# Optimization experiments

Measured on AMD Instinct MI355X. Metric: run time of the kernel, lower is better.

Reference implementation:

```python
import jax, jax.numpy as jnp
import numpy as np

B, T, C, N = 64, 2048, 1, 128  # batch, max seq len, num_conjugates, num_tags


def setup_inputs() -> dict:
    key = jax.random.key(0)
    k1, k2, k3, k4, k5 = jax.random.split(key, 5)
    emissions = jax.random.normal(k1, (B, T, C, N), dtype=jnp.float32)
    # ragged lengths in [T//2, T], guaranteed >= 1
    token_sizes = jax.random.randint(k2, (B,), T // 2, T + 1, dtype=jnp.int32)
    # learned CRF parameters (torch init is zeros; use small random for a nontrivial baseline)
    transitions = 0.1 * jax.random.normal(k3, (1, C, N, N), dtype=jnp.float32)
    head_transitions = 0.1 * jax.random.normal(k4, (1, C, N), dtype=jnp.float32)
    last_transitions = 0.1 * jax.random.normal(k5, (1, C, N), dtype=jnp.float32)
    return {
        "emissions": emissions,
        "token_sizes": token_sizes,
        "transitions": transitions,
        "head_transitions": head_transitions,
        "last_transitions": last_transitions,
    }


def _log_partition(emissions, transitions, head_transitions, last_transitions, token_sizes):
    # emissions: [B, T, C, N]; transitions: [1, C, N, N]; head/last: [1, C, N]
    trans = transitions[0]  # [C, N, N]
    # alpha_0 = head_transitions (*) emissions[0] in the Log semiring
    alpha0 = head_transitions[0][None, :, :] + emissions[:, 0]  # [B, C, N]

    def step(alpha, inp):
        em_t, t = inp  # em_t: [B, C, N], t: scalar time index
        # Log-semiring matmul: logsumexp over previous tag
        new = jax.nn.logsumexp(alpha[:, :, :, None] + trans[None, :, :, :], axis=2) + em_t
        valid = (t < token_sizes)[:, None, None]  # mask padded steps (identity in semiring)
        return jnp.where(valid, new, alpha), None

    step = jax.checkpoint(step)
    xs = (jnp.swapaxes(emissions[:, 1:], 0, 1), jnp.arange(1, emissions.shape[1]))
    alpha, _ = jax.lax.scan(step, alpha0, xs)
    # terminate with last_transitions, reduce over final tag
    return jax.nn.logsumexp(alpha + last_transitions[0][None, :, :], axis=-1)  # [B, C]


def reference(emissions, token_sizes, transitions, head_transitions, last_transitions):
    return _log_partition(emissions, transitions, head_transitions, last_transitions, token_sizes)
```

## Files before the change

### kernel.cpp

```cpp
#include <hip/hip_runtime.h>
#include <stdint.h>

#define T_LEN 2048
#define B_TOT 64
#define N_TAG 128
#define MID 1024

typedef __attribute__((ext_vector_type(4))) float f32x4;
typedef __attribute__((ext_vector_type(8))) short bf16x8;
typedef __attribute__((ext_vector_type(4))) uint32_t u32x4;
typedef __attribute__((ext_vector_type(2))) uint32_t u32x2;

template <int S>
struct IC {
  static constexpr int value = S;
};

__device__ __align__(16) float g_alpha[B_TOT][N_TAG];
__device__ __align__(16) float g_v[B_TOT][N_TAG];
__device__ float g_Lf[B_TOT];
__device__ float g_Lb[B_TOT];

__device__ __forceinline__ uint32_t pack2_bf16(float a, float b) {
  uint32_t ua = __float_as_uint(a) + 0x8000u;
  uint32_t ub = __float_as_uint(b) + 0x8000u;
  return __builtin_amdgcn_perm(ua, ub, 0x03020706u);
}
__device__ __forceinline__ float bf_lo(uint32_t w) {
  return __uint_as_float(w << 16);
}
__device__ __forceinline__ float bf_hi(uint32_t w) {
  return __uint_as_float(w & 0xffff0000u);
}

__global__ __launch_bounds__(256) void eem_prepass(const float* __restrict__ em,
                                                   uint32_t* __restrict__ ws) {
  const int tid = blockIdx.x * blockDim.x + threadIdx.x;
  const int b = tid >> 15;
  const int rem = tid & 32767;
  const int t = rem >> 4;
  const int kk = rem & 15;
  const float4* src =
      (const float4*)(em + ((size_t)b * T_LEN + t) * N_TAG + kk * 8);
  const float4 p0 = src[0];
  const float4 p1 = src[1];
  u32x4 o;
  o[0] = pack2_bf16(__expf(p0.x), __expf(p0.y));
  o[1] = pack2_bf16(__expf(p0.z), __expf(p0.w));
  o[2] = pack2_bf16(__expf(p1.x), __expf(p1.y));
  o[3] = pack2_bf16(__expf(p1.z), __expf(p1.w));
  *(u32x4*)(ws + ((size_t)t * B_TOT + b) * (N_TAG / 2) + kk * 4) = o;
}

__global__ __launch_bounds__(512, 2) void crf_scan_kernel(
    const float* __restrict__ em, const int* __restrict__ lens,
    const float* __restrict__ trans, const float* __restrict__ head,
    const float* __restrict__ last, const uint32_t* __restrict__ eem) {
  const int lane = threadIdx.x & 63;
  const int w = threadIdx.x >> 6;
  const int f = w >> 1;
  const int h = w & 1;
  const int c = lane & 15;
  const int q = lane >> 4;
  const bool is_fwd = (blockIdx.x < 4);
  const int bg = ((int)blockIdx.x & 3) * 16 + c;
  const int jbase = f * 32 + q * 8 + h * 4;

  __shared__ uint32_t x_lds[2][4][64][4];
  __shared__ int k_lds[16];

  const size_t eoff = (size_t)bg * 64 + f * 16 + q * 4 + h * 2;
  u32x2 eslot[4];
  auto issue_eem = [&](auto sc, int row) {
    constexpr int S = decltype(sc)::value;
    eslot[S] = *(const u32x2*)(eem + (size_t)row * 4096 + eoff);
  };

  const f32x4 vzero = {0.f, 0.f, 0.f, 0.f};

  if (is_fwd) {
    bf16x8 efrag[4];
    {
      const int j = f * 32 + (c >> 2) * 8 + h * 4 + (c & 3);
#pragma unroll
      for (int ktv = 0; ktv < 4; ++ktv) {
        const int ktp = (w + ktv) & 3;
        u32x4 wd;
#pragma unroll
        for (int p = 0; p < 4; ++p) {
          const int i0 = ktp * 32 + q * 8 + 2 * p;
          wd[p] = pack2_bf16(__expf(trans[(i0 + 0) * N_TAG + j]),
                             __expf(trans[(i0 + 1) * N_TAG + j]));
        }
        efrag[ktv] = __builtin_bit_cast(bf16x8, wd);
      }
    }
    float L = 0.f;
    const float* emb = em + (size_t)bg * T_LEN * N_TAG;
    {
      float v0[4];
#pragma unroll
      for (int r = 0; r < 4; ++r)
        v0[r] = __expf(head[jbase + r] + emb[jbase + r]);
      u32x2 wd;
      wd[0] = pack2_bf16(v0[0], v0[1]);
      wd[1] = pack2_bf16(v0[2], v0[3]);
      *(u32x2*)&x_lds[0][f][lane][h * 2] = wd;
    }
    if (w == 0 && lane < 16) k_lds[lane] = 0;
    __syncthreads();

    issue_eem(IC<1>{}, 1);
    issue_eem(IC<2>{}, 2);
    issue_eem(IC<3>{}, 3);

    auto step = [&](auto slotc, int t) {
      constexpr int SLOT = decltype(slotc)::value;
      constexpr int RP = (SLOT + 1) & 1;
      constexpr int WP = SLOT & 1;
      {
        int row = t + 3;
        if (row > T_LEN - 1) row = T_LEN - 1;
        issue_eem(IC<(SLOT + 3) & 3>{}, row);
      }
      int e = 0;
      if (SLOT == 1) e = k_lds[c];
      u32x4 bfr[4];
#pragma unroll
      for (int ktv = 0; ktv < 4; ++ktv)
        bfr[ktv] = *(const u32x4*)&x_lds[RP][(w + ktv) & 3][lane][0];
      const u32x2 ev = eslot[SLOT];
      float ff[4];
      ff[0] = bf_lo(ev[0]);
      ff[1] = bf_hi(ev[0]);
      ff[2] = bf_lo(ev[1]);
      ff[3] = bf_hi(ev[1]);
      if (SLOT == 1) {
        const float sc = __uint_as_float((uint32_t)(127 - e) << 23);
#pragma unroll
        for (int r = 0; r < 4; ++r) ff[r] *= sc;
        L += (float)e * 0.6931471805599453f;
      }
      f32x4 acc = __builtin_amdgcn_mfma_f32_16x16x32_bf16(
          efrag[0], __builtin_bit_cast(bf16x8, bfr[0]), vzero, 0, 0, 0);
      acc = __builtin_amdgcn_mfma_f32_16x16x32_bf16(
          efrag[1], __builtin_bit_cast(bf16x8, bfr[1]), acc, 0, 0, 0);
      acc = __builtin_amdgcn_mfma_f32_16x16x32_bf16(
          efrag[2], __builtin_bit_cast(bf16x8, bfr[2]), acc, 0, 0, 0);
      acc = __builtin_amdgcn_mfma_f32_16x16x32_bf16(
          efrag[3], __builtin_bit_cast(bf16x8, bfr[3]), acc, 0, 0, 0);
      if (SLOT == 0) {
        if (w == 0 && lane < 16)
          k_lds[c] = (int)(__float_as_uint(acc[0]) >> 23) - 126;
      }
      if (t == MID - 1) {
#pragma unroll
        for (int r = 0; r < 4; ++r) g_alpha[bg][jbase + r] = acc[r] * ff[r];
        if (w == 0 && q == 0) g_Lf[bg] = L;
      }
      u32x2 wd;
      wd[0] = pack2_bf16(acc[0] * ff[0], acc[1] * ff[1]);
      wd[1] = pack2_bf16(acc[2] * ff[2], acc[3] * ff[3]);
      *(u32x2*)&x_lds[WP][f][lane][h * 2] = wd;
      __syncthreads();
    };

    int t = 1;
#pragma unroll 1
    for (int it = 0; it < 255; ++it) {
      step(IC<1>{}, t);
      step(IC<2>{}, t + 1);
      step(IC<3>{}, t + 2);
      step(IC<0>{}, t + 3);
      t += 4;
    }
    step(IC<1>{}, t);
    step(IC<2>{}, t + 1);
    step(IC<3>{}, t + 2);
  } else {
    bf16x8 efrag[4];
    {
      const int irow = f * 32 + (c >> 2) * 8 + h * 4 + (c & 3);
#pragma unroll
      for (int ktv = 0; ktv < 4; ++ktv) {
        const int ktp = (w + ktv) & 3;
        u32x4 wd;
#pragma unroll
        for (int p = 0; p < 4; ++p) {
          const int j0 = ktp * 32 + q * 8 + 2 * p;
          wd[p] = pack2_bf16(__expf(trans[irow * N_TAG + j0 + 0]),
                             __expf(trans[irow * N_TAG + j0 + 1]));
        }
        efrag[ktv] = __builtin_bit_cast(bf16x8, wd);
      }
    }
    const int mylen = lens[bg];
    float L = 0.f;
    float vprev[4];
    {
      const u32x2 ev0 =
          *(const u32x2*)(eem + (size_t)(T_LEN - 1) * 4096 + eoff);
#pragma unroll
      for (int r = 0; r < 4; ++r) vprev[r] = __expf(last[jbase + r]);
      u32x2 wd;
      wd[0] = pack2_bf16(vprev[0] * bf_lo(ev0[0]), vprev[1] * bf_hi(ev0[0]));
      wd[1] = pack2_bf16(vprev[2] * bf_lo(ev0[1]), vprev[3] * bf_hi(ev0[1]));
      *(u32x2*)&x_lds[0][f][lane][h * 2] = wd;
    }
    if (w == 0 && lane < 16) k_lds[lane] = 0;
    __syncthreads();

    issue_eem(IC<1>{}, T_LEN - 2);
    issue_eem(IC<2>{}, T_LEN - 3);
    issue_eem(IC<3>{}, T_LEN - 4);

    auto step = [&](auto slotc, int t) {
      constexpr int SLOT = decltype(slotc)::value;
      constexpr int RP = (SLOT + 1) & 1;
      constexpr int WP = SLOT & 1;
      {
        int row = t - 4;
        if (row < 0) row = 0;
        issue_eem(IC<(SLOT + 3) & 3>{}, row);
      }
      int e = 0;
      if (SLOT == 1) e = k_lds[c];
      u32x4 bfr[4];
#pragma unroll
      for (int ktv = 0; ktv < 4; ++ktv)
        bfr[ktv] = *(const u32x4*)&x_lds[RP][(w + ktv) & 3][lane][0];
      const u32x2 ev = eslot[SLOT];
      float ee[4];
      ee[0] = bf_lo(ev[0]);
      ee[1] = bf_hi(ev[0]);
      ee[2] = bf_lo(ev[1]);
      ee[3] = bf_hi(ev[1]);
      f32x4 acc = __builtin_amdgcn_mfma_f32_16x16x32_bf16(
          efrag[0], __builtin_bit_cast(bf16x8, bfr[0]), vzero, 0, 0, 0);
      acc = __builtin_amdgcn_mfma_f32_16x16x32_bf16(
          efrag[1], __builtin_bit_cast(bf16x8, bfr[1]), acc, 0, 0, 0);
      acc = __builtin_amdgcn_mfma_f32_16x16x32_bf16(
          efrag[2], __builtin_bit_cast(bf16x8, bfr[2]), acc, 0, 0, 0);
      acc = __builtin_amdgcn_mfma_f32_16x16x32_bf16(
          efrag[3], __builtin_bit_cast(bf16x8, bfr[3]), acc, 0, 0, 0);
      const bool valid = (t < mylen);
      float vnew[4];
#pragma unroll
      for (int r = 0; r < 4; ++r) vnew[r] = valid ? acc[r] : vprev[r];
      if (SLOT == 1) {
        const float sc = __uint_as_float((uint32_t)(127 - e) << 23);
#pragma unroll
        for (int r = 0; r < 4; ++r) vnew[r] *= sc;
        L += (float)e * 0.6931471805599453f;
      }
      if (SLOT == 0) {
        if (w == 0 && lane < 16)
          k_lds[c] = (int)(__float_as_uint(vnew[0]) >> 23) - 126;
      }
      if (t == MID) {
#pragma unroll
        for (int r = 0; r < 4; ++r) g_v[bg][jbase + r] = vnew[r];
        if (w == 0 && q == 0) g_Lb[bg] = L;
      }
      u32x2 wd;
      wd[0] = pack2_bf16(vnew[0] * ee[0], vnew[1] * ee[1]);
      wd[1] = pack2_bf16(vnew[2] * ee[2], vnew[3] * ee[3]);
      *(u32x2*)&x_lds[WP][f][lane][h * 2] = wd;
#pragma unroll
      for (int r = 0; r < 4; ++r) vprev[r] = vnew[r];
      __syncthreads();
    };

    int t = T_LEN - 1;
#pragma unroll 1
    for (int it = 0; it < 256; ++it) {
      step(IC<1>{}, t);
      step(IC<2>{}, t - 1);
      step(IC<3>{}, t - 2);
      step(IC<0>{}, t - 3);
      t -= 4;
    }
  }
}

__global__ __launch_bounds__(256) void crf_combine(float* __restrict__ out) {
  const int tid = threadIdx.x;
  const int b = tid >> 2;
  const int p = tid & 3;
  float s = 0.f;
#pragma unroll
  for (int k = 0; k < 8; ++k) {
    const f32x4 a = *(const f32x4*)&g_alpha[b][p * 32 + k * 4];
    const f32x4 v = *(const f32x4*)&g_v[b][p * 32 + k * 4];
    s += a[0] * v[0] + a[1] * v[1] + a[2] * v[2] + a[3] * v[3];
  }
  s += __shfl_xor(s, 1);
  s += __shfl_xor(s, 2);
  if (p == 0) out[b] = __logf(s) + g_Lf[b] + g_Lb[b];
}

extern "C" void kernel_launch(void* const* d_in, const int* in_sizes, int n_in,
                              void* d_out, int out_size, void* d_ws,
                              size_t ws_size, hipStream_t stream) {
  const float* em = (const float*)d_in[0];
  const int* lens = (const int*)d_in[1];
  const float* trans = (const float*)d_in[2];
  const float* head = (const float*)d_in[3];
  const float* last = (const float*)d_in[4];
  float* out = (float*)d_out;
  uint32_t* ws = (uint32_t*)d_ws;

  eem_prepass<<<8192, 256, 0, stream>>>(em, ws);
  crf_scan_kernel<<<8, 512, 0, stream>>>(em, lens, trans, head, last, ws);
  crf_combine<<<1, 256, 0, stream>>>(out);
}
```

Before: 329.2 us.

## Fuse emission exp prepass into scan kernel and split MFMA accumulation chain

```diff
diff --git a/kernel.cpp b/kernel.cpp
--- a/kernel.cpp
+++ b/kernel.cpp
@@ -26,36 +26,11 @@
   uint32_t ub = __float_as_uint(b) + 0x8000u;
   return __builtin_amdgcn_perm(ua, ub, 0x03020706u);
 }
-__device__ __forceinline__ float bf_lo(uint32_t w) {
-  return __uint_as_float(w << 16);
-}
-__device__ __forceinline__ float bf_hi(uint32_t w) {
-  return __uint_as_float(w & 0xffff0000u);
-}
-
-__global__ __launch_bounds__(256) void eem_prepass(const float* __restrict__ em,
-                                                   uint32_t* __restrict__ ws) {
-  const int tid = blockIdx.x * blockDim.x + threadIdx.x;
-  const int b = tid >> 15;
-  const int rem = tid & 32767;
-  const int t = rem >> 4;
-  const int kk = rem & 15;
-  const float4* src =
-      (const float4*)(em + ((size_t)b * T_LEN + t) * N_TAG + kk * 8);
-  const float4 p0 = src[0];
-  const float4 p1 = src[1];
-  u32x4 o;
-  o[0] = pack2_bf16(__expf(p0.x), __expf(p0.y));
-  o[1] = pack2_bf16(__expf(p0.z), __expf(p0.w));
-  o[2] = pack2_bf16(__expf(p1.x), __expf(p1.y));
-  o[3] = pack2_bf16(__expf(p1.z), __expf(p1.w));
-  *(u32x4*)(ws + ((size_t)t * B_TOT + b) * (N_TAG / 2) + kk * 4) = o;
-}
 
 __global__ __launch_bounds__(512, 2) void crf_scan_kernel(
     const float* __restrict__ em, const int* __restrict__ lens,
     const float* __restrict__ trans, const float* __restrict__ head,
-    const float* __restrict__ last, const uint32_t* __restrict__ eem) {
+    const float* __restrict__ last) {
   const int lane = threadIdx.x & 63;
   const int w = threadIdx.x >> 6;
   const int f = w >> 1;
@@ -69,11 +44,11 @@
   __shared__ uint32_t x_lds[2][4][64][4];
   __shared__ int k_lds[16];
 
-  const size_t eoff = (size_t)bg * 64 + f * 16 + q * 4 + h * 2;
-  u32x2 eslot[4];
+  const float* eptr = em + (size_t)bg * T_LEN * N_TAG + jbase;
+  f32x4 eslot[4];
   auto issue_eem = [&](auto sc, int row) {
     constexpr int S = decltype(sc)::value;
-    eslot[S] = *(const u32x2*)(eem + (size_t)row * 4096 + eoff);
+    eslot[S] = *(const f32x4*)(eptr + (size_t)row * N_TAG);
   };
 
   const f32x4 vzero = {0.f, 0.f, 0.f, 0.f};
@@ -96,12 +71,10 @@
       }
     }
     float L = 0.f;
-    const float* emb = em + (size_t)bg * T_LEN * N_TAG;
     {
       float v0[4];
 #pragma unroll
-      for (int r = 0; r < 4; ++r)
-        v0[r] = __expf(head[jbase + r] + emb[jbase + r]);
+      for (int r = 0; r < 4; ++r) v0[r] = __expf(head[jbase + r] + eptr[r]);
       u32x2 wd;
       wd[0] = pack2_bf16(v0[0], v0[1]);
       wd[1] = pack2_bf16(v0[2], v0[3]);
@@ -129,26 +102,25 @@
 #pragma unroll
       for (int ktv = 0; ktv < 4; ++ktv)
         bfr[ktv] = *(const u32x4*)&x_lds[RP][(w + ktv) & 3][lane][0];
-      const u32x2 ev = eslot[SLOT];
+      const f32x4 ev = eslot[SLOT];
       float ff[4];
-      ff[0] = bf_lo(ev[0]);
-      ff[1] = bf_hi(ev[0]);
-      ff[2] = bf_lo(ev[1]);
-      ff[3] = bf_hi(ev[1]);
+#pragma unroll
+      for (int r = 0; r < 4; ++r) ff[r] = __expf(ev[r]);
       if (SLOT == 1) {
         const float sc = __uint_as_float((uint32_t)(127 - e) << 23);
 #pragma unroll
         for (int r = 0; r < 4; ++r) ff[r] *= sc;
         L += (float)e * 0.6931471805599453f;
       }
-      f32x4 acc = __builtin_amdgcn_mfma_f32_16x16x32_bf16(
+      f32x4 a0 = __builtin_amdgcn_mfma_f32_16x16x32_bf16(
           efrag[0], __builtin_bit_cast(bf16x8, bfr[0]), vzero, 0, 0, 0);
-      acc = __builtin_amdgcn_mfma_f32_16x16x32_bf16(
-          efrag[1], __builtin_bit_cast(bf16x8, bfr[1]), acc, 0, 0, 0);
-      acc = __builtin_amdgcn_mfma_f32_16x16x32_bf16(
-          efrag[2], __builtin_bit_cast(bf16x8, bfr[2]), acc, 0, 0, 0);
-      acc = __builtin_amdgcn_mfma_f32_16x16x32_bf16(
-          efrag[3], __builtin_bit_cast(bf16x8, bfr[3]), acc, 0, 0, 0);
+      f32x4 a1 = __builtin_amdgcn_mfma_f32_16x16x32_bf16(
+          efrag[2], __builtin_bit_cast(bf16x8, bfr[2]), vzero, 0, 0, 0);
+      a0 = __builtin_amdgcn_mfma_f32_16x16x32_bf16(
+          efrag[1], __builtin_bit_cast(bf16x8, bfr[1]), a0, 0, 0, 0);
+      a1 = __builtin_amdgcn_mfma_f32_16x16x32_bf16(
+          efrag[3], __builtin_bit_cast(bf16x8, bfr[3]), a1, 0, 0, 0);
+      const f32x4 acc = a0 + a1;
       if (SLOT == 0) {
         if (w == 0 && lane < 16)
           k_lds[c] = (int)(__float_as_uint(acc[0]) >> 23) - 126;
@@ -198,13 +170,15 @@
     float L = 0.f;
     float vprev[4];
     {
-      const u32x2 ev0 =
-          *(const u32x2*)(eem + (size_t)(T_LEN - 1) * 4096 + eoff);
 #pragma unroll
       for (int r = 0; r < 4; ++r) vprev[r] = __expf(last[jbase + r]);
-      u32x2 wd;
-      wd[0] = pack2_bf16(vprev[0] * bf_lo(ev0[0]), vprev[1] * bf_hi(ev0[0]));
-      wd[1] = pack2_bf16(vprev[2] * bf_lo(ev0[1]), vprev[3] * bf_hi(ev0[1]));
+      float e0[4];
+#pragma unroll
+      for (int r = 0; r < 4; ++r)
+        e0[r] = __expf(eptr[(size_t)(T_LEN - 1) * N_TAG + r]);
+      u32x2 wd;
+      wd[0] = pack2_bf16(vprev[0] * e0[0], vprev[1] * e0[1]);
+      wd[1] = pack2_bf16(vprev[2] * e0[2], vprev[3] * e0[3]);
       *(u32x2*)&x_lds[0][f][lane][h * 2] = wd;
     }
     if (w == 0 && lane < 16) k_lds[lane] = 0;
@@ -229,20 +203,19 @@
 #pragma unroll
       for (int ktv = 0; ktv < 4; ++ktv)
         bfr[ktv] = *(const u32x4*)&x_lds[RP][(w + ktv) & 3][lane][0];
-      const u32x2 ev = eslot[SLOT];
+      const f32x4 ev = eslot[SLOT];
       float ee[4];
-      ee[0] = bf_lo(ev[0]);
-      ee[1] = bf_hi(ev[0]);
-      ee[2] = bf_lo(ev[1]);
-      ee[3] = bf_hi(ev[1]);
-      f32x4 acc = __builtin_amdgcn_mfma_f32_16x16x32_bf16(
+#pragma unroll
+      for (int r = 0; r < 4; ++r) ee[r] = __expf(ev[r]);
+      f32x4 a0 = __builtin_amdgcn_mfma_f32_16x16x32_bf16(
           efrag[0], __builtin_bit_cast(bf16x8, bfr[0]), vzero, 0, 0, 0);
-      acc = __builtin_amdgcn_mfma_f32_16x16x32_bf16(
-          efrag[1], __builtin_bit_cast(bf16x8, bfr[1]), acc, 0, 0, 0);
-      acc = __builtin_amdgcn_mfma_f32_16x16x32_bf16(
-          efrag[2], __builtin_bit_cast(bf16x8, bfr[2]), acc, 0, 0, 0);
-      acc = __builtin_amdgcn_mfma_f32_16x16x32_bf16(
-          efrag[3], __builtin_bit_cast(bf16x8, bfr[3]), acc, 0, 0, 0);
+      f32x4 a1 = __builtin_amdgcn_mfma_f32_16x16x32_bf16(
+          efrag[2], __builtin_bit_cast(bf16x8, bfr[2]), vzero, 0, 0, 0);
+      a0 = __builtin_amdgcn_mfma_f32_16x16x32_bf16(
+          efrag[1], __builtin_bit_cast(bf16x8, bfr[1]), a0, 0, 0, 0);
+      a1 = __builtin_amdgcn_mfma_f32_16x16x32_bf16(
+          efrag[3], __builtin_bit_cast(bf16x8, bfr[3]), a1, 0, 0, 0);
+      const f32x4 acc = a0 + a1;
       const bool valid = (t < mylen);
       float vnew[4];
 #pragma unroll
@@ -308,9 +281,9 @@
   const float* head = (const float*)d_in[3];
   const float* last = (const float*)d_in[4];
   float* out = (float*)d_out;
-  uint32_t* ws = (uint32_t*)d_ws;
-
-  eem_prepass<<<8192, 256, 0, stream>>>(em, ws);
-  crf_scan_kernel<<<8, 512, 0, stream>>>(em, lens, trans, head, last, ws);
+  (void)d_ws;
+  (void)ws_size;
+
+  crf_scan_kernel<<<8, 512, 0, stream>>>(em, lens, trans, head, last);
   crf_combine<<<1, 256, 0, stream>>>(out);
 }
```

Result: no change. 335.6 us (+2.0%).

## Fuse combine into scan via ticket counter, lighter step barrier, split MFMA chain

Applied to the files above, without the earlier changes.

```diff
diff --git a/kernel.cpp b/kernel.cpp
--- a/kernel.cpp
+++ b/kernel.cpp
@@ -20,6 +20,7 @@
 __device__ __align__(16) float g_v[B_TOT][N_TAG];
 __device__ float g_Lf[B_TOT];
 __device__ float g_Lb[B_TOT];
+__device__ int g_done = 0;
 
 __device__ __forceinline__ uint32_t pack2_bf16(float a, float b) {
   uint32_t ua = __float_as_uint(a) + 0x8000u;
@@ -31,6 +32,14 @@
 }
 __device__ __forceinline__ float bf_hi(uint32_t w) {
   return __uint_as_float(w & 0xffff0000u);
+}
+
+__device__ __forceinline__ void step_barrier() {
+  __builtin_amdgcn_sched_barrier(0);
+  asm volatile("s_waitcnt lgkmcnt(0)");
+  __builtin_amdgcn_sched_barrier(0);
+  __builtin_amdgcn_s_barrier();
+  __builtin_amdgcn_sched_barrier(0);
 }
 
 __global__ __launch_bounds__(256) void eem_prepass(const float* __restrict__ em,
@@ -55,7 +64,8 @@
 __global__ __launch_bounds__(512, 2) void crf_scan_kernel(
     const float* __restrict__ em, const int* __restrict__ lens,
     const float* __restrict__ trans, const float* __restrict__ head,
-    const float* __restrict__ last, const uint32_t* __restrict__ eem) {
+    const float* __restrict__ last, const uint32_t* __restrict__ eem,
+    float* __restrict__ out) {
   const int lane = threadIdx.x & 63;
   const int w = threadIdx.x >> 6;
   const int f = w >> 1;
@@ -68,6 +78,7 @@
 
   __shared__ uint32_t x_lds[2][4][64][4];
   __shared__ int k_lds[16];
+  __shared__ int ticket_lds;
 
   const size_t eoff = (size_t)bg * 64 + f * 16 + q * 4 + h * 2;
   u32x2 eslot[4];
@@ -141,14 +152,15 @@
         for (int r = 0; r < 4; ++r) ff[r] *= sc;
         L += (float)e * 0.6931471805599453f;
       }
-      f32x4 acc = __builtin_amdgcn_mfma_f32_16x16x32_bf16(
+      f32x4 a0 = __builtin_amdgcn_mfma_f32_16x16x32_bf16(
           efrag[0], __builtin_bit_cast(bf16x8, bfr[0]), vzero, 0, 0, 0);
-      acc = __builtin_amdgcn_mfma_f32_16x16x32_bf16(
-          efrag[1], __builtin_bit_cast(bf16x8, bfr[1]), acc, 0, 0, 0);
-      acc = __builtin_amdgcn_mfma_f32_16x16x32_bf16(
-          efrag[2], __builtin_bit_cast(bf16x8, bfr[2]), acc, 0, 0, 0);
-      acc = __builtin_amdgcn_mfma_f32_16x16x32_bf16(
-          efrag[3], __builtin_bit_cast(bf16x8, bfr[3]), acc, 0, 0, 0);
+      f32x4 a1 = __builtin_amdgcn_mfma_f32_16x16x32_bf16(
+          efrag[2], __builtin_bit_cast(bf16x8, bfr[2]), vzero, 0, 0, 0);
+      a0 = __builtin_amdgcn_mfma_f32_16x16x32_bf16(
+          efrag[1], __builtin_bit_cast(bf16x8, bfr[1]), a0, 0, 0, 0);
+      a1 = __builtin_amdgcn_mfma_f32_16x16x32_bf16(
+          efrag[3], __builtin_bit_cast(bf16x8, bfr[3]), a1, 0, 0, 0);
+      const f32x4 acc = a0 + a1;
       if (SLOT == 0) {
         if (w == 0 && lane < 16)
           k_lds[c] = (int)(__float_as_uint(acc[0]) >> 23) - 126;
@@ -162,7 +174,7 @@
       wd[0] = pack2_bf16(acc[0] * ff[0], acc[1] * ff[1]);
       wd[1] = pack2_bf16(acc[2] * ff[2], acc[3] * ff[3]);
       *(u32x2*)&x_lds[WP][f][lane][h * 2] = wd;
-      __syncthreads();
+      step_barrier();
     };
 
     int t = 1;
@@ -235,14 +247,15 @@
       ee[1] = bf_hi(ev[0]);
       ee[2] = bf_lo(ev[1]);
       ee[3] = bf_hi(ev[1]);
-      f32x4 acc = __builtin_amdgcn_mfma_f32_16x16x32_bf16(
+      f32x4 a0 = __builtin_amdgcn_mfma_f32_16x16x32_bf16(
           efrag[0], __builtin_bit_cast(bf16x8, bfr[0]), vzero, 0, 0, 0);
-      acc = __builtin_amdgcn_mfma_f32_16x16x32_bf16(
-          efrag[1], __builtin_bit_cast(bf16x8, bfr[1]), acc, 0, 0, 0);
-      acc = __builtin_amdgcn_mfma_f32_16x16x32_bf16(
-          efrag[2], __builtin_bit_cast(bf16x8, bfr[2]), acc, 0, 0, 0);
-      acc = __builtin_amdgcn_mfma_f32_16x16x32_bf16(
-          efrag[3], __builtin_bit_cast(bf16x8, bfr[3]), acc, 0, 0, 0);
+      f32x4 a1 = __builtin_amdgcn_mfma_f32_16x16x32_bf16(
+          efrag[2], __builtin_bit_cast(bf16x8, bfr[2]), vzero, 0, 0, 0);
+      a0 = __builtin_amdgcn_mfma_f32_16x16x32_bf16(
+          efrag[1], __builtin_bit_cast(bf16x8, bfr[1]), a0, 0, 0, 0);
+      a1 = __builtin_amdgcn_mfma_f32_16x16x32_bf16(
+          efrag[3], __builtin_bit_cast(bf16x8, bfr[3]), a1, 0, 0, 0);
+      const f32x4 acc = a0 + a1;
       const bool valid = (t < mylen);
       float vnew[4];
 #pragma unroll
@@ -268,7 +281,7 @@
       *(u32x2*)&x_lds[WP][f][lane][h * 2] = wd;
 #pragma unroll
       for (int r = 0; r < 4; ++r) vprev[r] = vnew[r];
-      __syncthreads();
+      step_barrier();
     };
 
     int t = T_LEN - 1;
@@ -281,22 +294,28 @@
       t -= 4;
     }
   }
-}
-
-__global__ __launch_bounds__(256) void crf_combine(float* __restrict__ out) {
-  const int tid = threadIdx.x;
-  const int b = tid >> 2;
-  const int p = tid & 3;
-  float s = 0.f;
-#pragma unroll
-  for (int k = 0; k < 8; ++k) {
-    const f32x4 a = *(const f32x4*)&g_alpha[b][p * 32 + k * 4];
-    const f32x4 v = *(const f32x4*)&g_v[b][p * 32 + k * 4];
-    s += a[0] * v[0] + a[1] * v[1] + a[2] * v[2] + a[3] * v[3];
+
+  __threadfence();
+  if (threadIdx.x == 0) ticket_lds = atomicAdd(&g_done, 1);
+  __syncthreads();
+  if (ticket_lds == 7) {
+    __threadfence();
+    const int b = threadIdx.x >> 3;
+    const int p = threadIdx.x & 7;
+    float s = 0.f;
+#pragma unroll
+    for (int k = 0; k < 4; ++k) {
+      const f32x4 a = *(const f32x4*)&g_alpha[b][p * 16 + k * 4];
+      const f32x4 v = *(const f32x4*)&g_v[b][p * 16 + k * 4];
+      s += a[0] * v[0] + a[1] * v[1] + a[2] * v[2] + a[3] * v[3];
+    }
+    s += __shfl_xor(s, 1);
+    s += __shfl_xor(s, 2);
+    s += __shfl_xor(s, 4);
+    if (p == 0) out[b] = __logf(s) + g_Lf[b] + g_Lb[b];
+    __syncthreads();
+    if (threadIdx.x == 0) g_done = 0;
   }
-  s += __shfl_xor(s, 1);
-  s += __shfl_xor(s, 2);
-  if (p == 0) out[b] = __logf(s) + g_Lf[b] + g_Lb[b];
 }
 
 extern "C" void kernel_launch(void* const* d_in, const int* in_sizes, int n_in,
@@ -311,6 +330,5 @@
   uint32_t* ws = (uint32_t*)d_ws;
 
   eem_prepass<<<8192, 256, 0, stream>>>(em, ws);
-  crf_scan_kernel<<<8, 512, 0, stream>>>(em, lens, trans, head, last, ws);
-  crf_combine<<<1, 256, 0, stream>>>(out);
-}
+  crf_scan_kernel<<<8, 512, 0, stream>>>(em, lens, trans, head, last, ws, out);
+}
```

Result: slower. 355.6 us (+8.0%).
